# Optimization experiments

Hardware: AMD Instinct MI355X
Metric: run time of the kernel (lower is better)

## Reference

```python
import jax, jax.numpy as jnp
import numpy as np

LSTM_SIZE = 32
NUM_OPS = 64
NUM_EDGE = 128
TEMPERATURE = 5.0
TANH_CONST = 2.5


def _lstm_cell(x, h, c, W_ih, W_hh, b_ih, b_hh):
    # PyTorch gate order: i, f, g, o
    g = x @ W_ih.T + b_ih + h @ W_hh.T + b_hh  # [4*H]
    i, f, gg, o = jnp.split(g, 4)
    c2 = jax.nn.sigmoid(f) * c + jax.nn.sigmoid(i) * jnp.tanh(gg)
    h2 = jax.nn.sigmoid(o) * jnp.tanh(c2)
    return h2, c2


def setup_inputs() -> dict:
    key = jax.random.key(0)
    ks = jax.random.split(key, 12)
    H, G, O = LSTM_SIZE, 4 * LSTM_SIZE, NUM_OPS
    s = 0.1
    return {
        "input_vars": jax.random.uniform(ks[0], (1, 1, H), jnp.float32, -s, s),
        "W_ih0": jax.random.uniform(ks[1], (G, H), jnp.float32, -s, s),
        "W_hh0": jax.random.uniform(ks[2], (G, H), jnp.float32, -s, s),
        "b_ih0": jax.random.uniform(ks[3], (G,), jnp.float32, -s, s),
        "b_hh0": jax.random.uniform(ks[4], (G,), jnp.float32, -s, s),
        "W_ih1": jax.random.uniform(ks[5], (G, H), jnp.float32, -s, s),
        "W_hh1": jax.random.uniform(ks[6], (G, H), jnp.float32, -s, s),
        "b_ih1": jax.random.uniform(ks[7], (G,), jnp.float32, -s, s),
        "b_hh1": jax.random.uniform(ks[8], (G,), jnp.float32, -s, s),
        "embd": jax.random.uniform(ks[9], (O, H), jnp.float32, -s, s),
        "W_pred": jax.random.uniform(ks[10], (O, H), jnp.float32, -s, s),
        "b_pred": jax.random.uniform(ks[11], (O,), jnp.float32, -s, s),
        "num_edge": NUM_EDGE,
    }


def reference(input_vars, W_ih0, W_hh0, b_ih0, b_hh0,
              W_ih1, W_hh1, b_ih1, b_hh1,
              embd, W_pred, b_pred, num_edge):
    H = input_vars.shape[-1]
    x0 = input_vars.reshape(H)
    z = jnp.zeros((H,), input_vars.dtype)
    key0 = jax.random.key(42)

    def step(carry, _):
        key, x, h0, c0, h1, c1 = carry
        h0, c0 = _lstm_cell(x, h0, c0, W_ih0, W_hh0, b_ih0, b_hh0)
        h1, c1 = _lstm_cell(h0, h1, c1, W_ih1, W_hh1, b_ih1, b_hh1)
        logits = TANH_CONST * jnp.tanh((h1 @ W_pred.T + b_pred) / TEMPERATURE)
        key, sub = jax.random.split(key)
        idx = jax.random.categorical(sub, logits)
        logp = jax.nn.log_softmax(logits)
        lp = logp[idx]
        ent = -jnp.sum(jnp.exp(logp) * logp)
        x = embd[idx]
        return (key, x, h0, c0, h1, c1), (lp, ent, idx)

    _, (lps, ents, arch) = jax.lax.scan(step, (key0, x0, z, z, z, z), None, length=num_edge)
    return jnp.sum(lps), jnp.sum(ents), arch
```

## Files before the change

### kernel.cpp

```cpp
#include <hip/hip_runtime.h>
#include <stdint.h>

namespace {

typedef float v2f __attribute__((ext_vector_type(2)));
typedef int   v2i __attribute__((ext_vector_type(2)));

constexpr int H      = 32;
constexpr int NEDGE  = 128;
constexpr float TINY   = 1.1754943508222875e-38f;
constexpr float L2E    = 1.4426950408889634f;
constexpr float LN2    = 0.6931471805599453f;

__device__ __forceinline__ void tf_round(uint32_t& x0, uint32_t& x1, int r) {
  x0 += x1;
  x1 = (x1 << r) | (x1 >> (32 - r));
  x1 ^= x0;
}

__device__ __forceinline__ void tf2x32(uint32_t k0, uint32_t k1,
                                       uint32_t& x0, uint32_t& x1) {
  const uint32_t ks2 = k0 ^ k1 ^ 0x1BD11BDAu;
  x0 += k0; x1 += k1;
  tf_round(x0,x1,13); tf_round(x0,x1,15); tf_round(x0,x1,26); tf_round(x0,x1, 6);
  x0 += k1;  x1 += ks2 + 1u;
  tf_round(x0,x1,17); tf_round(x0,x1,29); tf_round(x0,x1,16); tf_round(x0,x1,24);
  x0 += ks2; x1 += k0 + 2u;
  tf_round(x0,x1,13); tf_round(x0,x1,15); tf_round(x0,x1,26); tf_round(x0,x1, 6);
  x0 += k0;  x1 += k1 + 3u;
  tf_round(x0,x1,17); tf_round(x0,x1,29); tf_round(x0,x1,16); tf_round(x0,x1,24);
  x0 += k1;  x1 += ks2 + 4u;
  tf_round(x0,x1,13); tf_round(x0,x1,15); tf_round(x0,x1,26); tf_round(x0,x1, 6);
  x0 += ks2; x1 += k0 + 5u;
}

__device__ __forceinline__ float fexp(float x) {
  return __builtin_amdgcn_exp2f(x * L2E);
}
__device__ __forceinline__ float flog(float x) {
  return __builtin_amdgcn_logf(x) * LN2;
}
__device__ __forceinline__ float fsigmoid(float x) {
  return __builtin_amdgcn_rcpf(1.0f + __builtin_amdgcn_exp2f(-x * L2E));
}
__device__ __forceinline__ float ftanh(float x) {
  const float ax = __builtin_fabsf(x);
  const float t  = __builtin_amdgcn_exp2f(ax * (-2.0f * L2E));
  const float r  = (1.0f - t) * __builtin_amdgcn_rcpf(1.0f + t);
  return __builtin_copysignf(r, x);
}

__device__ __forceinline__ float rdlane(float v, int i) {
  return __int_as_float(__builtin_amdgcn_readlane(__float_as_int(v), i));
}

template <int CTRL>
__device__ __forceinline__ float dppf(float v) {
  return __int_as_float(__builtin_amdgcn_update_dpp(
      __float_as_int(v), __float_as_int(v), CTRL, 0xF, 0xF, false));
}

__device__ __forceinline__ float wave_sum64(float v) {
  v += dppf<0xB1>(v);
  v += dppf<0x4E>(v);
  v += dppf<0x141>(v);
  v += dppf<0x140>(v);
  return (rdlane(v, 15) + rdlane(v, 31)) + (rdlane(v, 47) + rdlane(v, 63));
}

__device__ __forceinline__ float wave_max64(float v) {
  v = fmaxf(v, dppf<0xB1>(v));
  v = fmaxf(v, dppf<0x4E>(v));
  v = fmaxf(v, dppf<0x141>(v));
  v = fmaxf(v, dppf<0x140>(v));
  return fmaxf(fmaxf(rdlane(v, 15), rdlane(v, 31)),
               fmaxf(rdlane(v, 47), rdlane(v, 63)));
}

__device__ __forceinline__ v2f pkfma(v2f a, v2f b, v2f c) {
  return __builtin_elementwise_fma(a, b, c);
}

__device__ __forceinline__ v2f permswap_pair(float g) {
  const v2i r = __builtin_amdgcn_permlane32_swap(
      __float_as_int(g), __float_as_int(g), false, false);
  return v2f{__int_as_float(r.x), __int_as_float(r.y)};
}

__global__ __launch_bounds__(192, 1)
void ctrl_kernel(const float* __restrict__ input_vars,
                 const float* __restrict__ W_ih0, const float* __restrict__ W_hh0,
                 const float* __restrict__ b_ih0, const float* __restrict__ b_hh0,
                 const float* __restrict__ W_ih1, const float* __restrict__ W_hh1,
                 const float* __restrict__ b_ih1, const float* __restrict__ b_hh1,
                 const float* __restrict__ embd,
                 const float* __restrict__ W_pred, const float* __restrict__ b_pred,
                 float* __restrict__ out) {
  const int tid  = threadIdx.x;
  const int lane = tid & 63;
  const int wid  = tid >> 6;
  const int rB   = lane + 64;

  __shared__ __align__(16) float embd_lds[65 * H];
  __shared__ __align__(16) float h0buf[2][H];
  __shared__ __align__(16) float gumbuf[4][64];
  __shared__ __align__(16) float xbuf[2][H];
  __shared__ __align__(16) float arch_lds[NEDGE];

  if (wid < 2) {
#pragma unroll
    for (int j = 0; j < 4; ++j)
      reinterpret_cast<float4*>(embd_lds)[(tid & 127) + 128 * j] =
          reinterpret_cast<const float4*>(embd)[(tid & 127) + 128 * j];
    if (tid < 8)
      reinterpret_cast<float4*>(&embd_lds[64 * H])[tid] =
          reinterpret_cast<const float4*>(input_vars)[tid];
    if (tid < 8)
      reinterpret_cast<float4*>(&xbuf[0][0])[tid] =
          reinterpret_cast<const float4*>(input_vars)[tid];
  }

  const float* WX = (wid == 1) ? W_ih1 : W_ih0;
  const float* WH = (wid == 1) ? W_hh1 : W_hh0;
  float4 wxA[8], wxB[8], whA[8], whB[8];
#pragma unroll
  for (int q = 0; q < 8; ++q) {
    wxA[q] = reinterpret_cast<const float4*>(WX + lane * H)[q];
    wxB[q] = reinterpret_cast<const float4*>(WX + rB * H)[q];
    whA[q] = reinterpret_cast<const float4*>(WH + lane * H)[q];
    whB[q] = reinterpret_cast<const float4*>(WH + rB * H)[q];
  }
  float4 wp4[8];
  if (wid == 1) {
#pragma unroll
    for (int q = 0; q < 8; ++q)
      wp4[q] = reinterpret_cast<const float4*>(W_pred + lane * H)[q];
  }
  const float bsum0A = b_ih0[lane] + b_hh0[lane];
  const float bsum0B = b_ih0[rB]   + b_hh0[rB];
  const float bsum1A = b_ih1[lane] + b_hh1[lane];
  const float bsum1B = b_ih1[rB]   + b_hh1[rB];
  const float bp = b_pred[lane];

  float c0 = 0.f, h0v = 0.f;
  float c1 = 0.f, h1v = 0.f;
  v2f hoA01={0.f,0.f}, hoA23={0.f,0.f}, hoB01={0.f,0.f}, hoB23={0.f,0.f};
  uint32_t k0 = 0u, k1 = 42u;
  uint32_t s0c = 0u, s1c = 0u;
  float lp_sum = 0.f, ent_sum = 0.f;
  float logit_prev = 0.f;
  int   idx_prev = 0;

  if (wid == 2) {
#pragma unroll 1
    for (int p = 0; p < 2; ++p) {
      uint32_t r0 = 0u, r1 = (uint32_t)(lane & 1);
      tf2x32(k0, k1, r0, r1);
      const uint32_t n0 = (uint32_t)__builtin_amdgcn_readlane((int)r0, 0);
      const uint32_t n1 = (uint32_t)__builtin_amdgcn_readlane((int)r1, 0);
      const uint32_t s0 = (uint32_t)__builtin_amdgcn_readlane((int)r0, 1);
      const uint32_t s1 = (uint32_t)__builtin_amdgcn_readlane((int)r1, 1);
      uint32_t x0 = 0u, x1 = (uint32_t)lane;
      tf2x32(s0, s1, x0, x1);
      const uint32_t bits = x0 ^ x1;
      k0 = n0; k1 = n1;
      float u = __uint_as_float(0x3f800000u | (bits >> 9)) - 1.0f;
      u = fmaxf(u + TINY, TINY);
      gumbuf[p][lane] = -flog(-flog(u));
    }
  }
  __syncthreads();

  for (int t = 0; t < NEDGE; ++t) {
    v2f rA01={0.f,0.f}, rA23={0.f,0.f}, rB01={0.f,0.f}, rB23={0.f,0.f};

    if (wid == 0) {
      v2f xA01={0.f,0.f}, xA23={0.f,0.f}, xB01={0.f,0.f}, xB23={0.f,0.f};
#pragma unroll
      for (int q = 0; q < 8; ++q) {
        const float4 x4 =
            *reinterpret_cast<const float4*>(&xbuf[t & 1][4 * q]);
        xA01 = pkfma(v2f{x4.x, x4.y}, v2f{wxA[q].x, wxA[q].y}, xA01);
        xA23 = pkfma(v2f{x4.z, x4.w}, v2f{wxA[q].z, wxA[q].w}, xA23);
        xB01 = pkfma(v2f{x4.x, x4.y}, v2f{wxB[q].x, wxB[q].y}, xB01);
        xB23 = pkfma(v2f{x4.z, x4.w}, v2f{wxB[q].z, wxB[q].w}, xB23);
      }
      const float gA = bsum0A + ((xA01.x + xA01.y) + (xA23.x + xA23.y))
                              + ((hoA01.x + hoA01.y) + (hoA23.x + hoA23.y));
      const float gB = bsum0B + ((xB01.x + xB01.y) + (xB23.x + xB23.y))
                              + ((hoB01.x + hoB01.y) + (hoB23.x + hoB23.y));
      const v2f gif = permswap_pair(gA);
      const v2f ggo = permswap_pair(gB);
      c0 = fsigmoid(gif.y) * c0 + fsigmoid(gif.x) * ftanh(ggo.x);
      h0v = fsigmoid(ggo.y) * ftanh(c0);
      h0buf[t & 1][lane & 31] = h0v;
    } else if (wid == 1) {
#pragma unroll
      for (int q = 0; q < 8; ++q) {
        const v2f h01 = {rdlane(h1v, 4*q+0), rdlane(h1v, 4*q+1)};
        const v2f h23 = {rdlane(h1v, 4*q+2), rdlane(h1v, 4*q+3)};
        rA01 = pkfma(h01, v2f{whA[q].x, whA[q].y}, rA01);
        rA23 = pkfma(h23, v2f{whA[q].z, whA[q].w}, rA23);
        rB01 = pkfma(h01, v2f{whB[q].x, whB[q].y}, rB01);
        rB23 = pkfma(h23, v2f{whB[q].z, whB[q].w}, rB23);
      }
      if (t > 0) {
        const float e  = fexp(logit_prev);
        const float E  = wave_sum64(e);
        const float ES = wave_sum64(e * logit_prev);
        const float lse = flog(E);
        const float li  = rdlane(logit_prev, idx_prev);
        lp_sum  += li - lse;
        ent_sum += lse - ES / E;
      }
    } else {
      uint32_t r0 = 0u, r1 = (uint32_t)(lane & 1);
      tf2x32(k0, k1, r0, r1);
      k0  = (uint32_t)__builtin_amdgcn_readlane((int)r0, 0);
      k1  = (uint32_t)__builtin_amdgcn_readlane((int)r1, 0);
      s0c = (uint32_t)__builtin_amdgcn_readlane((int)r0, 1);
      s1c = (uint32_t)__builtin_amdgcn_readlane((int)r1, 1);
    }
    __syncthreads();

    if (wid == 0) {
      hoA01 = v2f{0.f,0.f}; hoA23 = v2f{0.f,0.f};
      hoB01 = v2f{0.f,0.f}; hoB23 = v2f{0.f,0.f};
#pragma unroll
      for (int q = 0; q < 8; ++q) {
        const v2f h01 = {rdlane(h0v, 4*q+0), rdlane(h0v, 4*q+1)};
        const v2f h23 = {rdlane(h0v, 4*q+2), rdlane(h0v, 4*q+3)};
        hoA01 = pkfma(h01, v2f{whA[q].x, whA[q].y}, hoA01);
        hoA23 = pkfma(h23, v2f{whA[q].z, whA[q].w}, hoA23);
        hoB01 = pkfma(h01, v2f{whB[q].x, whB[q].y}, hoB01);
        hoB23 = pkfma(h23, v2f{whB[q].z, whB[q].w}, hoB23);
      }
    } else if (wid == 1) {
#pragma unroll
      for (int q = 0; q < 8; ++q) {
        const float4 h4 =
            *reinterpret_cast<const float4*>(&h0buf[t & 1][4 * q]);
        rA01 = pkfma(v2f{h4.x, h4.y}, v2f{wxA[q].x, wxA[q].y}, rA01);
        rA23 = pkfma(v2f{h4.z, h4.w}, v2f{wxA[q].z, wxA[q].w}, rA23);
        rB01 = pkfma(v2f{h4.x, h4.y}, v2f{wxB[q].x, wxB[q].y}, rB01);
        rB23 = pkfma(v2f{h4.z, h4.w}, v2f{wxB[q].z, wxB[q].w}, rB23);
      }
      const float gA1 = bsum1A + ((rA01.x + rA01.y) + (rA23.x + rA23.y));
      const float gB1 = bsum1B + ((rB01.x + rB01.y) + (rB23.x + rB23.y));
      const v2f gif1 = permswap_pair(gA1);
      const v2f ggo1 = permswap_pair(gB1);
      c1  = fsigmoid(gif1.y) * c1 + fsigmoid(gif1.x) * ftanh(ggo1.x);
      h1v = fsigmoid(ggo1.y) * ftanh(c1);

      v2f p01 = {0.f, 0.f}, p23 = {0.f, 0.f};
#pragma unroll
      for (int q = 0; q < 8; ++q) {
        const float4 w = wp4[q];
        p01 = pkfma(v2f{rdlane(h1v, 4*q+0), rdlane(h1v, 4*q+1)},
                    v2f{w.x, w.y}, p01);
        p23 = pkfma(v2f{rdlane(h1v, 4*q+2), rdlane(h1v, 4*q+3)},
                    v2f{w.z, w.w}, p23);
      }
      const float pre   = bp + ((p01.x + p01.y) + (p23.x + p23.y));
      const float logit = 2.5f * ftanh(pre * 0.2f);
      const float pert  = logit + gumbuf[t & 3][lane];

      const float M = wave_max64(pert);
      const unsigned long long msk = __ballot(pert == M);
      const int idxu = __ffsll((long long)msk) - 1;

      arch_lds[t] = (float)idxu;
      logit_prev = logit;
      idx_prev   = idxu;
      xbuf[(t + 1) & 1][lane & 31] = embd_lds[idxu * H + (lane & 31)];
    } else {
      uint32_t x0 = 0u, x1 = (uint32_t)lane;
      tf2x32(s0c, s1c, x0, x1);
      const uint32_t bits = x0 ^ x1;
      float u = __uint_as_float(0x3f800000u | (bits >> 9)) - 1.0f;
      u = fmaxf(u + TINY, TINY);
      gumbuf[(t + 2) & 3][lane] = -flog(-flog(u));
    }
    __syncthreads();
  }

  if (wid == 1) {
    const float e  = fexp(logit_prev);
    const float E  = wave_sum64(e);
    const float ES = wave_sum64(e * logit_prev);
    const float lse = flog(E);
    const float li  = rdlane(logit_prev, idx_prev);
    lp_sum  += li - lse;
    ent_sum += lse - ES / E;

    out[2 + lane]      = arch_lds[lane];
    out[2 + 64 + lane] = arch_lds[64 + lane];
    if (lane == 0) { out[0] = lp_sum; out[1] = ent_sum; }
  }
}

}

extern "C" void kernel_launch(void* const* d_in, const int* in_sizes, int n_in,
                              void* d_out, int out_size, void* d_ws, size_t ws_size,
                              hipStream_t stream) {
  (void)in_sizes; (void)n_in; (void)d_ws; (void)ws_size; (void)out_size;
  const float* input_vars = (const float*)d_in[0];
  const float* W_ih0 = (const float*)d_in[1];
  const float* W_hh0 = (const float*)d_in[2];
  const float* b_ih0 = (const float*)d_in[3];
  const float* b_hh0 = (const float*)d_in[4];
  const float* W_ih1 = (const float*)d_in[5];
  const float* W_hh1 = (const float*)d_in[6];
  const float* b_ih1 = (const float*)d_in[7];
  const float* b_hh1 = (const float*)d_in[8];
  const float* embd  = (const float*)d_in[9];
  const float* W_pred = (const float*)d_in[10];
  const float* b_pred = (const float*)d_in[11];
  float* out = (float*)d_out;

  hipLaunchKernelGGL(ctrl_kernel, dim3(1), dim3(192), 0, stream,
                     input_vars, W_ih0, W_hh0, b_ih0, b_hh0,
                     W_ih1, W_hh1, b_ih1, b_hh1,
                     embd, W_pred, b_pred, out);
}
```

Baseline: 130.5 us.

## Precompute embedding input projections and pipeline layer-0/layer-1 with flag handoff

Wave 0 precomputes W_ih0·x for all 64 embeddings plus the initial input into a shared table before the loop, so each step's input projection becomes a table lookup chosen by the sampled index. The recurrence is restructured into a skewed pipeline: layer 1 for step s and layer 0 for step s+1 run in the same iteration, with the sampled row passed through a shared-memory flag spin-wait instead of an extra barrier. This drops one __syncthreads per step and shortens the critical path, but adds a spin-wait between waves in the same block and roughly 33KB more LDS.

Measured after the change: 135.7 us. 1.04x slower.

```diff
diff --git a/kernel.cpp b/kernel.cpp
--- a/kernel.cpp
+++ b/kernel.cpp
@@ -102,10 +102,14 @@
   const int rB   = lane + 64;
 
   __shared__ __align__(16) float embd_lds[65 * H];
+  __shared__ __align__(16) float xdot[65][128];
   __shared__ __align__(16) float h0buf[2][H];
   __shared__ __align__(16) float gumbuf[4][64];
-  __shared__ __align__(16) float xbuf[2][H];
+  __shared__ __align__(16) float xfer[2][2][64];
   __shared__ __align__(16) float arch_lds[NEDGE];
+  __shared__ int w1flag;
+
+  if (tid == 0) w1flag = 0;
 
   if (wid < 2) {
 #pragma unroll
@@ -115,9 +119,6 @@
     if (tid < 8)
       reinterpret_cast<float4*>(&embd_lds[64 * H])[tid] =
           reinterpret_cast<const float4*>(input_vars)[tid];
-    if (tid < 8)
-      reinterpret_cast<float4*>(&xbuf[0][0])[tid] =
-          reinterpret_cast<const float4*>(input_vars)[tid];
   }
 
   const float* WX = (wid == 1) ? W_ih1 : W_ih0;
@@ -142,18 +143,11 @@
   const float bsum1B = b_ih1[rB]   + b_hh1[rB];
   const float bp = b_pred[lane];
 
-  float c0 = 0.f, h0v = 0.f;
-  float c1 = 0.f, h1v = 0.f;
-  v2f hoA01={0.f,0.f}, hoA23={0.f,0.f}, hoB01={0.f,0.f}, hoB23={0.f,0.f};
   uint32_t k0 = 0u, k1 = 42u;
   uint32_t s0c = 0u, s1c = 0u;
-  float lp_sum = 0.f, ent_sum = 0.f;
-  float logit_prev = 0.f;
-  int   idx_prev = 0;
 
   if (wid == 2) {
-#pragma unroll 1
-    for (int p = 0; p < 2; ++p) {
+    {
       uint32_t r0 = 0u, r1 = (uint32_t)(lane & 1);
       tf2x32(k0, k1, r0, r1);
       const uint32_t n0 = (uint32_t)__builtin_amdgcn_readlane((int)r0, 0);
@@ -166,35 +160,133 @@
       k0 = n0; k1 = n1;
       float u = __uint_as_float(0x3f800000u | (bits >> 9)) - 1.0f;
       u = fmaxf(u + TINY, TINY);
-      gumbuf[p][lane] = -flog(-flog(u));
+      gumbuf[0][lane] = -flog(-flog(u));
+    }
+    {
+      uint32_t r0 = 0u, r1 = (uint32_t)(lane & 1);
+      tf2x32(k0, k1, r0, r1);
+      k0  = (uint32_t)__builtin_amdgcn_readlane((int)r0, 0);
+      k1  = (uint32_t)__builtin_amdgcn_readlane((int)r1, 0);
+      s0c = (uint32_t)__builtin_amdgcn_readlane((int)r0, 1);
+      s1c = (uint32_t)__builtin_amdgcn_readlane((int)r1, 1);
     }
   }
   __syncthreads();
 
-  for (int t = 0; t < NEDGE; ++t) {
-    v2f rA01={0.f,0.f}, rA23={0.f,0.f}, rB01={0.f,0.f}, rB23={0.f,0.f};
-
-    if (wid == 0) {
+#define W2_STEP(GIDX)                                                       \
+  {                                                                         \
+    uint32_t x0 = 0u, x1 = (uint32_t)lane;                                  \
+    tf2x32(s0c, s1c, x0, x1);                                               \
+    const uint32_t bits = x0 ^ x1;                                          \
+    float u = __uint_as_float(0x3f800000u | (bits >> 9)) - 1.0f;            \
+    u = fmaxf(u + TINY, TINY);                                              \
+    gumbuf[(GIDX) & 3][lane] = -flog(-flog(u));                             \
+    uint32_t r0 = 0u, r1 = (uint32_t)(lane & 1);                            \
+    tf2x32(k0, k1, r0, r1);                                                 \
+    k0  = (uint32_t)__builtin_amdgcn_readlane((int)r0, 0);                  \
+    k1  = (uint32_t)__builtin_amdgcn_readlane((int)r1, 0);                  \
+    s0c = (uint32_t)__builtin_amdgcn_readlane((int)r0, 1);                  \
+    s1c = (uint32_t)__builtin_amdgcn_readlane((int)r1, 1);                  \
+  }
+
+  if (wid == 0) {
+    for (int op = 0; op < 65; ++op) {
       v2f xA01={0.f,0.f}, xA23={0.f,0.f}, xB01={0.f,0.f}, xB23={0.f,0.f};
 #pragma unroll
       for (int q = 0; q < 8; ++q) {
         const float4 x4 =
-            *reinterpret_cast<const float4*>(&xbuf[t & 1][4 * q]);
+            *reinterpret_cast<const float4*>(&embd_lds[op * H + 4 * q]);
         xA01 = pkfma(v2f{x4.x, x4.y}, v2f{wxA[q].x, wxA[q].y}, xA01);
         xA23 = pkfma(v2f{x4.z, x4.w}, v2f{wxA[q].z, wxA[q].w}, xA23);
         xB01 = pkfma(v2f{x4.x, x4.y}, v2f{wxB[q].x, wxB[q].y}, xB01);
         xB23 = pkfma(v2f{x4.z, x4.w}, v2f{wxB[q].z, wxB[q].w}, xB23);
       }
-      const float gA = bsum0A + ((xA01.x + xA01.y) + (xA23.x + xA23.y))
-                              + ((hoA01.x + hoA01.y) + (hoA23.x + hoA23.y));
-      const float gB = bsum0B + ((xB01.x + xB01.y) + (xB23.x + xB23.y))
-                              + ((hoB01.x + hoB01.y) + (hoB23.x + hoB23.y));
-      const v2f gif = permswap_pair(gA);
-      const v2f ggo = permswap_pair(gB);
-      c0 = fsigmoid(gif.y) * c0 + fsigmoid(gif.x) * ftanh(ggo.x);
-      h0v = fsigmoid(ggo.y) * ftanh(c0);
-      h0buf[t & 1][lane & 31] = h0v;
-    } else if (wid == 1) {
+      xdot[op][lane] = (xA01.x + xA01.y) + (xA23.x + xA23.y);
+      xdot[op][rB]   = (xB01.x + xB01.y) + (xB23.x + xB23.y);
+    }
+  } else if (wid == 2) {
+    W2_STEP(1)
+  }
+  __syncthreads();
+
+  float c0 = 0.f, h0v = 0.f;
+  v2f hoA01={0.f,0.f}, hoA23={0.f,0.f}, hoB01={0.f,0.f}, hoB23={0.f,0.f};
+  if (wid == 0) {
+    const float xdA = xdot[64][lane];
+    const float xdB = xdot[64][rB];
+    const float gA = (bsum0A + xdA)
+                   + ((hoA01.x + hoA01.y) + (hoA23.x + hoA23.y));
+    const float gB = (bsum0B + xdB)
+                   + ((hoB01.x + hoB01.y) + (hoB23.x + hoB23.y));
+    const v2f gif = permswap_pair(gA);
+    const v2f ggo = permswap_pair(gB);
+    c0 = fsigmoid(gif.y) * c0 + fsigmoid(gif.x) * ftanh(ggo.x);
+    h0v = fsigmoid(ggo.y) * ftanh(c0);
+    h0buf[0][lane & 31] = h0v;
+#pragma unroll
+    for (int q = 0; q < 8; ++q) {
+      const v2f h01 = {rdlane(h0v, 4*q+0), rdlane(h0v, 4*q+1)};
+      const v2f h23 = {rdlane(h0v, 4*q+2), rdlane(h0v, 4*q+3)};
+      hoA01 = pkfma(h01, v2f{whA[q].x, whA[q].y}, hoA01);
+      hoA23 = pkfma(h23, v2f{whA[q].z, whA[q].w}, hoA23);
+      hoB01 = pkfma(h01, v2f{whB[q].x, whB[q].y}, hoB01);
+      hoB23 = pkfma(h23, v2f{whB[q].z, whB[q].w}, hoB23);
+    }
+  } else if (wid == 2) {
+    W2_STEP(2)
+  }
+  __syncthreads();
+
+  float c1 = 0.f, h1v = 0.f;
+  v2f rA01={0.f,0.f}, rA23={0.f,0.f}, rB01={0.f,0.f}, rB23={0.f,0.f};
+  float lp_sum = 0.f, ent_sum = 0.f;
+  float logit_prev = 0.f;
+  int   idx_prev = 0;
+
+  for (int p = 2; p <= 129; ++p) {
+    if (wid == 1) {
+      const int s = p - 2;
+#pragma unroll
+      for (int q = 0; q < 8; ++q) {
+        const float4 h4 =
+            *reinterpret_cast<const float4*>(&h0buf[s & 1][4 * q]);
+        rA01 = pkfma(v2f{h4.x, h4.y}, v2f{wxA[q].x, wxA[q].y}, rA01);
+        rA23 = pkfma(v2f{h4.z, h4.w}, v2f{wxA[q].z, wxA[q].w}, rA23);
+        rB01 = pkfma(v2f{h4.x, h4.y}, v2f{wxB[q].x, wxB[q].y}, rB01);
+        rB23 = pkfma(v2f{h4.z, h4.w}, v2f{wxB[q].z, wxB[q].w}, rB23);
+      }
+      const float gA1 = bsum1A + ((rA01.x + rA01.y) + (rA23.x + rA23.y));
+      const float gB1 = bsum1B + ((rB01.x + rB01.y) + (rB23.x + rB23.y));
+      const v2f gif1 = permswap_pair(gA1);
+      const v2f ggo1 = permswap_pair(gB1);
+      c1  = fsigmoid(gif1.y) * c1 + fsigmoid(gif1.x) * ftanh(ggo1.x);
+      h1v = fsigmoid(ggo1.y) * ftanh(c1);
+
+      v2f p01 = {0.f, 0.f}, p23 = {0.f, 0.f};
+#pragma unroll
+      for (int q = 0; q < 8; ++q) {
+        const float4 w = wp4[q];
+        p01 = pkfma(v2f{rdlane(h1v, 4*q+0), rdlane(h1v, 4*q+1)},
+                    v2f{w.x, w.y}, p01);
+        p23 = pkfma(v2f{rdlane(h1v, 4*q+2), rdlane(h1v, 4*q+3)},
+                    v2f{w.z, w.w}, p23);
+      }
+      const float pre   = bp + ((p01.x + p01.y) + (p23.x + p23.y));
+      const float logit = 2.5f * ftanh(pre * 0.2f);
+      const float pert  = logit + gumbuf[s & 3][lane];
+
+      const float M = wave_max64(pert);
+      const unsigned long long msk = __ballot(pert == M);
+      const int idxu = __ffsll((long long)msk) - 1;
+
+      arch_lds[s] = (float)idxu;
+      xfer[s & 1][0][lane] = xdot[idxu][lane];
+      xfer[s & 1][1][lane] = xdot[idxu][rB];
+      __threadfence_block();
+      *(volatile int*)&w1flag = s + 1;
+
+      rA01 = v2f{0.f,0.f}; rA23 = v2f{0.f,0.f};
+      rB01 = v2f{0.f,0.f}; rB23 = v2f{0.f,0.f};
 #pragma unroll
       for (int q = 0; q < 8; ++q) {
         const v2f h01 = {rdlane(h1v, 4*q+0), rdlane(h1v, 4*q+1)};
@@ -204,7 +296,7 @@
         rB01 = pkfma(h01, v2f{whB[q].x, whB[q].y}, rB01);
         rB23 = pkfma(h23, v2f{whB[q].z, whB[q].w}, rB23);
       }
-      if (t > 0) {
+      if (s > 0) {
         const float e  = fexp(logit_prev);
         const float E  = wave_sum64(e);
         const float ES = wave_sum64(e * logit_prev);
@@ -213,76 +305,41 @@
         lp_sum  += li - lse;
         ent_sum += lse - ES / E;
       }
-    } else {
-      uint32_t r0 = 0u, r1 = (uint32_t)(lane & 1);
-      tf2x32(k0, k1, r0, r1);
-      k0  = (uint32_t)__builtin_amdgcn_readlane((int)r0, 0);
-      k1  = (uint32_t)__builtin_amdgcn_readlane((int)r1, 0);
-      s0c = (uint32_t)__builtin_amdgcn_readlane((int)r0, 1);
-      s1c = (uint32_t)__builtin_amdgcn_readlane((int)r1, 1);
-    }
-    __syncthreads();
-
-    if (wid == 0) {
-      hoA01 = v2f{0.f,0.f}; hoA23 = v2f{0.f,0.f};
-      hoB01 = v2f{0.f,0.f}; hoB23 = v2f{0.f,0.f};
-#pragma unroll
-      for (int q = 0; q < 8; ++q) {
-        const v2f h01 = {rdlane(h0v, 4*q+0), rdlane(h0v, 4*q+1)};
-        const v2f h23 = {rdlane(h0v, 4*q+2), rdlane(h0v, 4*q+3)};
-        hoA01 = pkfma(h01, v2f{whA[q].x, whA[q].y}, hoA01);
-        hoA23 = pkfma(h23, v2f{whA[q].z, whA[q].w}, hoA23);
-        hoB01 = pkfma(h01, v2f{whB[q].x, whB[q].y}, hoB01);
-        hoB23 = pkfma(h23, v2f{whB[q].z, whB[q].w}, hoB23);
-      }
-    } else if (wid == 1) {
-#pragma unroll
-      for (int q = 0; q < 8; ++q) {
-        const float4 h4 =
-            *reinterpret_cast<const float4*>(&h0buf[t & 1][4 * q]);
-        rA01 = pkfma(v2f{h4.x, h4.y}, v2f{wxA[q].x, wxA[q].y}, rA01);
-        rA23 = pkfma(v2f{h4.z, h4.w}, v2f{wxA[q].z, wxA[q].w}, rA23);
-        rB01 = pkfma(v2f{h4.x, h4.y}, v2f{wxB[q].x, wxB[q].y}, rB01);
-        rB23 = pkfma(v2f{h4.z, h4.w}, v2f{wxB[q].z, wxB[q].w}, rB23);
-      }
-      const float gA1 = bsum1A + ((rA01.x + rA01.y) + (rA23.x + rA23.y));
-      const float gB1 = bsum1B + ((rB01.x + rB01.y) + (rB23.x + rB23.y));
-      const v2f gif1 = permswap_pair(gA1);
-      const v2f ggo1 = permswap_pair(gB1);
-      c1  = fsigmoid(gif1.y) * c1 + fsigmoid(gif1.x) * ftanh(ggo1.x);
-      h1v = fsigmoid(ggo1.y) * ftanh(c1);
-
-      v2f p01 = {0.f, 0.f}, p23 = {0.f, 0.f};
-#pragma unroll
-      for (int q = 0; q < 8; ++q) {
-        const float4 w = wp4[q];
-        p01 = pkfma(v2f{rdlane(h1v, 4*q+0), rdlane(h1v, 4*q+1)},
-                    v2f{w.x, w.y}, p01);
-        p23 = pkfma(v2f{rdlane(h1v, 4*q+2), rdlane(h1v, 4*q+3)},
-                    v2f{w.z, w.w}, p23);
-      }
-      const float pre   = bp + ((p01.x + p01.y) + (p23.x + p23.y));
-      const float logit = 2.5f * ftanh(pre * 0.2f);
-      const float pert  = logit + gumbuf[t & 3][lane];
-
-      const float M = wave_max64(pert);
-      const unsigned long long msk = __ballot(pert == M);
-      const int idxu = __ffsll((long long)msk) - 1;
-
-      arch_lds[t] = (float)idxu;
       logit_prev = logit;
       idx_prev   = idxu;
-      xbuf[(t + 1) & 1][lane & 31] = embd_lds[idxu * H + (lane & 31)];
+    } else if (wid == 0) {
+      if (p <= 128) {
+        while (*(volatile int*)&w1flag < p - 1) {}
+        __threadfence_block();
+        const float xdA = xfer[(p - 2) & 1][0][lane];
+        const float xdB = xfer[(p - 2) & 1][1][lane];
+        const float gA = (bsum0A + xdA)
+                       + ((hoA01.x + hoA01.y) + (hoA23.x + hoA23.y));
+        const float gB = (bsum0B + xdB)
+                       + ((hoB01.x + hoB01.y) + (hoB23.x + hoB23.y));
+        const v2f gif = permswap_pair(gA);
+        const v2f ggo = permswap_pair(gB);
+        c0 = fsigmoid(gif.y) * c0 + fsigmoid(gif.x) * ftanh(ggo.x);
+        h0v = fsigmoid(ggo.y) * ftanh(c0);
+        h0buf[(p - 1) & 1][lane & 31] = h0v;
+        hoA01 = v2f{0.f,0.f}; hoA23 = v2f{0.f,0.f};
+        hoB01 = v2f{0.f,0.f}; hoB23 = v2f{0.f,0.f};
+#pragma unroll
+        for (int q = 0; q < 8; ++q) {
+          const v2f h01 = {rdlane(h0v, 4*q+0), rdlane(h0v, 4*q+1)};
+          const v2f h23 = {rdlane(h0v, 4*q+2), rdlane(h0v, 4*q+3)};
+          hoA01 = pkfma(h01, v2f{whA[q].x, whA[q].y}, hoA01);
+          hoA23 = pkfma(h23, v2f{whA[q].z, whA[q].w}, hoA23);
+          hoB01 = pkfma(h01, v2f{whB[q].x, whB[q].y}, hoB01);
+          hoB23 = pkfma(h23, v2f{whB[q].z, whB[q].w}, hoB23);
+        }
+      }
     } else {
-      uint32_t x0 = 0u, x1 = (uint32_t)lane;
-      tf2x32(s0c, s1c, x0, x1);
-      const uint32_t bits = x0 ^ x1;
-      float u = __uint_as_float(0x3f800000u | (bits >> 9)) - 1.0f;
-      u = fmaxf(u + TINY, TINY);
-      gumbuf[(t + 2) & 3][lane] = -flog(-flog(u));
+      if (p <= 126) W2_STEP(p + 1)
     }
     __syncthreads();
   }
+#undef W2_STEP
 
   if (wid == 1) {
     const float e  = fexp(logit_prev);
```

## Precompute input projections for all embeddings and move softmax stats to RNG wave

Applied to the files above, without the earlier changes.

Before the recurrence, wave 0 computes W_ih0·x for all 64 embedding rows plus the initial input and stores them in LDS. Each step then gathers the selected row's precomputed gate contribution, which removes the per-step input matvec from the serial chain. The log-softmax and entropy accumulation moves from wave 1 to the otherwise lightly loaded RNG wave, reading logits through LDS. The cost is a one-off prologue and about 33KB of extra LDS.

Measured after the change: 128.6 us (median of 2 runs). About the same (-1.5%).

```diff
diff --git a/kernel.cpp b/kernel.cpp
--- a/kernel.cpp
+++ b/kernel.cpp
@@ -102,9 +102,11 @@
   const int rB   = lane + 64;
 
   __shared__ __align__(16) float embd_lds[65 * H];
+  __shared__ __align__(16) float xdot[65][128];
   __shared__ __align__(16) float h0buf[2][H];
   __shared__ __align__(16) float gumbuf[4][64];
-  __shared__ __align__(16) float xbuf[2][H];
+  __shared__ __align__(16) float xfer[2][2][64];
+  __shared__ __align__(16) float logitbuf[2][64];
   __shared__ __align__(16) float arch_lds[NEDGE];
 
   if (wid < 2) {
@@ -115,9 +117,6 @@
     if (tid < 8)
       reinterpret_cast<float4*>(&embd_lds[64 * H])[tid] =
           reinterpret_cast<const float4*>(input_vars)[tid];
-    if (tid < 8)
-      reinterpret_cast<float4*>(&xbuf[0][0])[tid] =
-          reinterpret_cast<const float4*>(input_vars)[tid];
   }
 
   const float* WX = (wid == 1) ? W_ih1 : W_ih0;
@@ -148,8 +147,6 @@
   uint32_t k0 = 0u, k1 = 42u;
   uint32_t s0c = 0u, s1c = 0u;
   float lp_sum = 0.f, ent_sum = 0.f;
-  float logit_prev = 0.f;
-  int   idx_prev = 0;
 
   if (wid == 2) {
 #pragma unroll 1
@@ -171,24 +168,34 @@
   }
   __syncthreads();
 
-  for (int t = 0; t < NEDGE; ++t) {
-    v2f rA01={0.f,0.f}, rA23={0.f,0.f}, rB01={0.f,0.f}, rB23={0.f,0.f};
-
-    if (wid == 0) {
+  if (wid == 0) {
+    for (int op = 0; op < 65; ++op) {
       v2f xA01={0.f,0.f}, xA23={0.f,0.f}, xB01={0.f,0.f}, xB23={0.f,0.f};
 #pragma unroll
       for (int q = 0; q < 8; ++q) {
         const float4 x4 =
-            *reinterpret_cast<const float4*>(&xbuf[t & 1][4 * q]);
+            *reinterpret_cast<const float4*>(&embd_lds[op * H + 4 * q]);
         xA01 = pkfma(v2f{x4.x, x4.y}, v2f{wxA[q].x, wxA[q].y}, xA01);
         xA23 = pkfma(v2f{x4.z, x4.w}, v2f{wxA[q].z, wxA[q].w}, xA23);
         xB01 = pkfma(v2f{x4.x, x4.y}, v2f{wxB[q].x, wxB[q].y}, xB01);
         xB23 = pkfma(v2f{x4.z, x4.w}, v2f{wxB[q].z, wxB[q].w}, xB23);
       }
-      const float gA = bsum0A + ((xA01.x + xA01.y) + (xA23.x + xA23.y))
-                              + ((hoA01.x + hoA01.y) + (hoA23.x + hoA23.y));
-      const float gB = bsum0B + ((xB01.x + xB01.y) + (xB23.x + xB23.y))
-                              + ((hoB01.x + hoB01.y) + (hoB23.x + hoB23.y));
+      xdot[op][lane] = (xA01.x + xA01.y) + (xA23.x + xA23.y);
+      xdot[op][rB]   = (xB01.x + xB01.y) + (xB23.x + xB23.y);
+    }
+  }
+  __syncthreads();
+
+  for (int t = 0; t < NEDGE; ++t) {
+    v2f rA01={0.f,0.f}, rA23={0.f,0.f}, rB01={0.f,0.f}, rB23={0.f,0.f};
+
+    if (wid == 0) {
+      const float xdA = (t == 0) ? xdot[64][lane] : xfer[t & 1][0][lane];
+      const float xdB = (t == 0) ? xdot[64][rB]   : xfer[t & 1][1][lane];
+      const float gA = (bsum0A + xdA)
+                     + ((hoA01.x + hoA01.y) + (hoA23.x + hoA23.y));
+      const float gB = (bsum0B + xdB)
+                     + ((hoB01.x + hoB01.y) + (hoB23.x + hoB23.y));
       const v2f gif = permswap_pair(gA);
       const v2f ggo = permswap_pair(gB);
       c0 = fsigmoid(gif.y) * c0 + fsigmoid(gif.x) * ftanh(ggo.x);
@@ -203,15 +210,6 @@
         rA23 = pkfma(h23, v2f{whA[q].z, whA[q].w}, rA23);
         rB01 = pkfma(h01, v2f{whB[q].x, whB[q].y}, rB01);
         rB23 = pkfma(h23, v2f{whB[q].z, whB[q].w}, rB23);
-      }
-      if (t > 0) {
-        const float e  = fexp(logit_prev);
-        const float E  = wave_sum64(e);
-        const float ES = wave_sum64(e * logit_prev);
-        const float lse = flog(E);
-        const float li  = rdlane(logit_prev, idx_prev);
-        lp_sum  += li - lse;
-        ent_sum += lse - ES / E;
       }
     } else {
       uint32_t r0 = 0u, r1 = (uint32_t)(lane & 1);
@@ -270,9 +268,9 @@
       const int idxu = __ffsll((long long)msk) - 1;
 
       arch_lds[t] = (float)idxu;
-      logit_prev = logit;
-      idx_prev   = idxu;
-      xbuf[(t + 1) & 1][lane & 31] = embd_lds[idxu * H + (lane & 31)];
+      logitbuf[t & 1][lane] = logit;
+      xfer[(t + 1) & 1][0][lane] = xdot[idxu][lane];
+      xfer[(t + 1) & 1][1][lane] = xdot[idxu][rB];
     } else {
       uint32_t x0 = 0u, x1 = (uint32_t)lane;
       tf2x32(s0c, s1c, x0, x1);
@@ -280,22 +278,35 @@
       float u = __uint_as_float(0x3f800000u | (bits >> 9)) - 1.0f;
       u = fmaxf(u + TINY, TINY);
       gumbuf[(t + 2) & 3][lane] = -flog(-flog(u));
+      if (t > 0) {
+        const float lg  = logitbuf[(t - 1) & 1][lane];
+        const int  idxp = (int)arch_lds[t - 1];
+        const float e  = fexp(lg);
+        const float E  = wave_sum64(e);
+        const float ES = wave_sum64(e * lg);
+        const float lse = flog(E);
+        const float li  = logitbuf[(t - 1) & 1][idxp];
+        lp_sum  += li - lse;
+        ent_sum += lse - ES / E;
+      }
     }
     __syncthreads();
   }
 
-  if (wid == 1) {
-    const float e  = fexp(logit_prev);
+  if (wid == 2) {
+    const float lg  = logitbuf[127 & 1][lane];
+    const int  idxp = (int)arch_lds[127];
+    const float e  = fexp(lg);
     const float E  = wave_sum64(e);
-    const float ES = wave_sum64(e * logit_prev);
+    const float ES = wave_sum64(e * lg);
     const float lse = flog(E);
-    const float li  = rdlane(logit_prev, idx_prev);
+    const float li  = logitbuf[127 & 1][idxp];
     lp_sum  += li - lse;
     ent_sum += lse - ES / E;
-
+    if (lane == 0) { out[0] = lp_sum; out[1] = ent_sum; }
+  } else if (wid == 1) {
     out[2 + lane]      = arch_lds[lane];
     out[2 + 64 + lane] = arch_lds[64 + lane];
-    if (lane == 0) { out[0] = lp_sum; out[1] = ent_sum; }
   }
 }
 
```
